# Kernel optimization log

Hardware: AMD Instinct MI355X
Metric: run time of the kernel (lower is better)

## Reference

```python
import jax, jax.numpy as jnp
import numpy as np

NUM_HEADS = 16


def setup_inputs() -> dict:
    key = jax.random.key(0)
    ks = jax.random.split(key, 8)
    b, n, m, L, d = 2, 1024, 4, 1024, 1024
    x = jax.random.normal(ks[0], (b, n, d), dtype=jnp.float32)
    context = jax.random.normal(ks[1], (b, m, L, d), dtype=jnp.float32)
    doc_similarities = jax.random.normal(ks[2], (b, m), dtype=jnp.float32)
    mask = jnp.ones((b, n), dtype=bool)
    context_mask = jnp.ones((b, m, L), dtype=bool)
    Wq = jax.random.normal(ks[3], (d, d), dtype=jnp.float32) * 0.02
    Wkv = jax.random.normal(ks[4], (d, 2 * d), dtype=jnp.float32) * 0.02
    Wout = jax.random.normal(ks[5], (d, d), dtype=jnp.float32) * 0.02
    bout = jnp.zeros((d,), dtype=jnp.float32)
    beta = jnp.ones((), dtype=jnp.float32)
    return {"x": x, "context": context, "doc_similarities": doc_similarities,
            "mask": mask, "context_mask": context_mask,
            "Wq": Wq, "Wkv": Wkv, "Wout": Wout, "bout": bout, "beta": beta}


def reference(x, context, doc_similarities, mask, context_mask, Wq, Wkv, Wout, bout, beta):
    b, n, d = x.shape
    h = NUM_HEADS
    hd = d // h
    _, m, L, _ = context.shape
    kv_len = m * L

    # q projection -> (b, h, n, hd)
    q = (x @ Wq).reshape(b, n, h, hd).transpose(0, 2, 1, 3)

    ctx = context.reshape(b, kv_len, d)
    cmask = context_mask.reshape(b, kv_len)

    # doc similarity bias, broadcast per-token within each doc, scaled by beta
    ds = jnp.repeat(doc_similarities[:, :, None], L, axis=-1).reshape(b, kv_len)
    ds = ds[:, None, None, :] * beta  # (b, 1, 1, kv_len)

    kv = ctx @ Wkv  # (b, kv_len, 2d)
    k, v = jnp.split(kv, 2, axis=-1)
    k = k.reshape(b, kv_len, h, hd).transpose(0, 2, 3, 1)  # (b, h, hd, kv_len)
    v = v.reshape(b, kv_len, h, hd).transpose(0, 2, 1, 3)  # (b, h, kv_len, hd)

    # NOTE: original scales by d**-0.5 (full model dim), not head_size**-0.5
    attention_pre_doc_sim = (q @ k) * (d ** -0.5)  # (b, h, n, kv_len)
    attention = attention_pre_doc_sim + ds

    # faithful mask path: multiply by cross mask, then map exact zeros to -inf
    cross_mask = mask[:, None, :, None] * cmask[:, None, None, :]  # (b,1,n,kv_len)
    attention = attention * cross_mask
    attention = jnp.where(attention == 0.0, -jnp.inf, attention)

    attention_weights = jax.nn.softmax(attention, axis=-1)
    # dropout_rate = 0.0 -> identity

    out = (attention_weights @ v).transpose(0, 2, 1, 3).reshape(b, n, d)
    out = out @ Wout + bout
    return out, attention_pre_doc_sim
```

## Files before the change

kernel.cpp:

```cpp
#include <hip/hip_runtime.h>
#include <cstdint>
#include <cstddef>

typedef unsigned short u16t;
typedef __attribute__((ext_vector_type(4))) float f32x4;
typedef __attribute__((ext_vector_type(4))) int i32x4;
typedef __attribute__((ext_vector_type(8))) __bf16 bf16x8;
typedef __attribute__((ext_vector_type(4))) __bf16 bf16x4;
typedef __attribute__((ext_vector_type(8))) unsigned short u16x8;
typedef __attribute__((ext_vector_type(4))) unsigned short u16x4;

#define INFF __builtin_inff()

__device__ __forceinline__ u16t f2b(float f) {
  union { float f; unsigned u; } x; x.f = f;
  unsigned r = x.u + 0x7FFFu + ((x.u >> 16) & 1u);
  return (u16t)(r >> 16);
}

__device__ __forceinline__ void gload16(const u16t* g, u16t* l) {
  __builtin_amdgcn_global_load_lds((const __attribute__((address_space(1))) void*)g,
                                   (__attribute__((address_space(3))) void*)l, 16, 0, 0);
}

__global__ __launch_bounds__(256) void k_prep(const float* __restrict__ x,
                                              const float* __restrict__ ctx,
                                              u16t* __restrict__ x16,
                                              u16t* __restrict__ ctx16,
                                              const int* __restrict__ cmask,
                                              const float* __restrict__ dsim,
                                              const float* __restrict__ beta_p,
                                              float* __restrict__ biasf) {
  const int bx = blockIdx.x, tid = threadIdx.x;
  if (bx < 2048) {
    int i = bx * 256 + tid;
    f32x4 v = *(const f32x4*)(x + (size_t)i * 4);
    u16x4 o;
    o[0] = f2b(v[0]); o[1] = f2b(v[1]); o[2] = f2b(v[2]); o[3] = f2b(v[3]);
    *(u16x4*)(x16 + (size_t)i * 4) = o;
  } else if (bx < 10240) {
    int i = (bx - 2048) * 256 + tid;
    f32x4 v = *(const f32x4*)(ctx + (size_t)i * 4);
    u16x4 o;
    o[0] = f2b(v[0]); o[1] = f2b(v[1]); o[2] = f2b(v[2]); o[3] = f2b(v[3]);
    *(u16x4*)(ctx16 + (size_t)i * 4) = o;
  } else {
    int idx = (bx - 10240) * 256 + tid;
    int c = idx * 4;
    const float beta = beta_p[0];
    const float ds = dsim[(c >> 12) * 4 + ((c & 4095) >> 10)] * beta;
    i32x4 cm = *(const i32x4*)(cmask + c);
    f32x4 bv;
#pragma unroll
    for (int j = 0; j < 4; ++j) bv[j] = cm[j] ? ds : -INFF;
    *(f32x4*)(biasf + c) = bv;
  }
}

__global__ __launch_bounds__(256) void k_transpose_w3(const float* __restrict__ Wq,
                                                      const float* __restrict__ Wkv,
                                                      const float* __restrict__ Wout,
                                                      u16t* __restrict__ WqT,
                                                      u16t* __restrict__ WkvT,
                                                      u16t* __restrict__ WoutT) {
  __shared__ float tile[64 * 65];
  const int t = threadIdx.x;
  const int bxx = blockIdx.x;
  const float* src; u16t* dst; int C, cb;
  if (bxx < 16)      { src = Wq;   dst = WqT;   C = 1024; cb = bxx * 64; }
  else if (bxx < 48) { src = Wkv;  dst = WkvT;  C = 2048; cb = (bxx - 16) * 64; }
  else               { src = Wout; dst = WoutT; C = 1024; cb = (bxx - 48) * 64; }
  const int rb = blockIdx.y * 64;
#pragma unroll
  for (int it = 0; it < 4; ++it) {
    int c = it * 256 + t;
    int r = c >> 4, ch = c & 15;
    f32x4 v = *(const f32x4*)(src + (size_t)(rb + r) * C + cb + ch * 4);
    float* dp = &tile[r * 65 + ch * 4];
    dp[0] = v[0]; dp[1] = v[1]; dp[2] = v[2]; dp[3] = v[3];
  }
  __syncthreads();
#pragma unroll
  for (int it = 0; it < 2; ++it) {
    int c = it * 256 + t;
    int dr = c >> 3, ch = c & 7;
    u16x8 o;
#pragma unroll
    for (int i = 0; i < 8; ++i) o[i] = f2b(tile[(ch * 8 + i) * 65 + dr]);
    *(u16x8*)(dst + (size_t)(cb + dr) * 1024 + rb + ch * 8) = o;
  }
}

template <int MODE>
__global__ __launch_bounds__(256) void k_gemm_bt(const u16t* __restrict__ A,
                                                 const u16t* __restrict__ Bt,
                                                 void* __restrict__ C,
                                                 u16t* __restrict__ C2,
                                                 const float* __restrict__ bias,
                                                 float oscale,
                                                 int K, int lda, int ldb, int ldc, int nbx) {
  __shared__ u16t As[128 * 64];
  __shared__ u16t Bs[128 * 64];
  const int tid = threadIdx.x;
  const int lane = tid & 63, wid = tid >> 6;
  const int l16 = lane & 15, lg = lane >> 4;
  const int wr = wid >> 1, wc = wid & 1;
  const int g = blockIdx.x, per = gridDim.x >> 3;
  const int w = (g & 7) * per + (g >> 3);
  const int bx = w % nbx, by = w / nbx;
  const int brow = by * 128, bcol = bx * 128;
  const int sr = lane >> 3, chs = lane & 7;
  f32x4 acc[4][4] = {};

  for (int k0 = 0; k0 < K; k0 += 64) {
#pragma unroll
    for (int it = 0; it < 4; ++it) {
      int row = it * 32 + wid * 8 + sr;
      int ch = chs ^ (row & 7);
      gload16(A + (size_t)(brow + row) * lda + k0 + ch * 8, &As[it * 2048 + wid * 512]);
      gload16(Bt + (size_t)(bcol + row) * ldb + k0 + ch * 8, &Bs[it * 2048 + wid * 512]);
    }
    __syncthreads();
#pragma unroll
    for (int kk = 0; kk < 2; ++kk) {
      bf16x8 af[4], bfv[4];
#pragma unroll
      for (int mi = 0; mi < 4; ++mi) {
        int row = wr * 64 + mi * 16 + l16;
        int kch = (kk * 4 + lg) ^ (row & 7);
        af[mi] = *(const bf16x8*)(&As[row * 64 + kch * 8]);
      }
#pragma unroll
      for (int ni = 0; ni < 4; ++ni) {
        int row = wc * 64 + ni * 16 + l16;
        int kch = (kk * 4 + lg) ^ (row & 7);
        bfv[ni] = *(const bf16x8*)(&Bs[row * 64 + kch * 8]);
      }
#pragma unroll
      for (int mi = 0; mi < 4; ++mi)
#pragma unroll
        for (int ni = 0; ni < 4; ++ni)
          acc[mi][ni] = __builtin_amdgcn_mfma_f32_16x16x32_bf16(af[mi], bfv[ni], acc[mi][ni], 0, 0, 0);
    }
    __syncthreads();
  }

  if (MODE == 2 && bcol >= 1024) {
#pragma unroll
    for (int mi = 0; mi < 4; ++mi) {
#pragma unroll
      for (int ni = 0; ni < 4; ++ni) {
        int vcol = bcol - 1024 + wc * 64 + ni * 16 + l16;
        int h = vcol >> 6, hd = vcol & 63;
        int row0 = brow + wr * 64 + mi * 16 + lg * 4;
        int bb = row0 >> 12, pos = row0 & 4095;
        u16x4 o4;
#pragma unroll
        for (int j = 0; j < 4; ++j) o4[j] = f2b(acc[mi][ni][j]);
        *(u16x4*)(C2 + ((size_t)((bb * 16 + h) * 64 + hd)) * 4096 + pos) = o4;
      }
    }
    return;
  }
#pragma unroll
  for (int mi = 0; mi < 4; ++mi) {
#pragma unroll
    for (int ni = 0; ni < 4; ++ni) {
#pragma unroll
      for (int j = 0; j < 4; ++j) {
        size_t row = (size_t)brow + wr * 64 + mi * 16 + lg * 4 + j;
        int col = bcol + wc * 64 + ni * 16 + l16;
        float v = acc[mi][ni][j] * oscale;
        if (MODE == 1) {
          v += bias[col];
          __builtin_nontemporal_store(v, (float*)C + row * ldc + col);
        } else {
          ((u16t*)C)[row * ldc + col] = f2b(v);
        }
      }
    }
  }
}

__global__ __launch_bounds__(256) void k_attn(const u16t* __restrict__ k16,
                                              const u16t* __restrict__ vT16,
                                              const u16t* __restrict__ q16,
                                              const float* __restrict__ biasf,
                                              const int* __restrict__ mask,
                                              float* __restrict__ pre,
                                              u16t* __restrict__ O16) {
  __shared__ u16t Ks[2][128 * 64];
  __shared__ u16t Vs[2][64 * 128];
  __shared__ u16t Ps[4 * 16 * 128];

  const int tid = threadIdx.x;
  const int lane = tid & 63, wid = tid >> 6;
  const int l16 = lane & 15, lg = lane >> 4;
  const int g = blockIdx.x;
  const int w = (g & 7) * 64 + (g >> 3);
  const int nb = w & 15, hb = w >> 4;
  const int h = hb & 15, b = hb >> 4;
  const int qrow0 = nb * 64 + wid * 16;

  bf16x8 aq0, aq1;
  {
    const u16t* qp = q16 + (size_t)(b * 1024 + qrow0 + l16) * 1024 + h * 64 + lg * 8;
    aq0 = *(const bf16x8*)(qp);
    aq1 = *(const bf16x8*)(qp + 32);
  }
  const bool qm = mask[b * 1024 + qrow0 + l16] != 0;

  float mrow = -INFF, lsum = 0.f;
  f32x4 o[4] = {};

  const u16t* kbase = k16 + (size_t)b * 4096 * 1024 + (size_t)h * 64;
  const u16t* vbase = vT16 + (size_t)(b * 16 + h) * 64 * 4096;
  float* prerow = pre + (size_t)((b * 16 + h) * 1024 + qrow0 + l16) * 4096;
  const float* biasb = biasf + b * 4096;
  u16t* Pw = &Ps[wid * 2048];
  char* Pwb = (char*)Pw + l16 * 256;
  const int pswz = (l16 & 7) << 4;

  auto stage = [&](int bufi, int kv0s) {
    u16t* Kb = &Ks[bufi][wid * 2048];
    u16t* Vb = &Vs[bufi][wid * 2048];
#pragma unroll
    for (int it = 0; it < 4; ++it) {
      int row = wid * 32 + it * 8 + (lane >> 3);
      int ch = (lane & 7) ^ (row & 7);
      gload16(kbase + (size_t)(kv0s + row) * 1024 + ch * 8, Kb + it * 512);
    }
#pragma unroll
    for (int it = 0; it < 4; ++it) {
      int row = wid * 16 + it * 4 + (lane >> 4);
      int ch = (lane & 15) ^ (row & 7);
      gload16(vbase + (size_t)row * 4096 + kv0s + ch * 8, Vb + it * 512);
    }
  };

  int cur = 0;
  stage(0, 0);
  __syncthreads();

  for (int t = 0; t < 32; ++t) {
    if (t + 1 < 32) stage(cur ^ 1, (t + 1) * 128);
    asm volatile("" ::: "memory");
    const u16t* Kc = &Ks[cur][0];
    const u16t* Vc = &Vs[cur][0];
    const int kv0 = t * 128;

    f32x4 s[8];
#pragma unroll
    for (int kb = 0; kb < 8; ++kb) {
      f32x4 acc = {0.f, 0.f, 0.f, 0.f};
      int row = kb * 16 + l16;
      bf16x8 bk0 = *(const bf16x8*)(&Kc[row * 64 + ((lg ^ (row & 7)) << 3)]);
      bf16x8 bk1 = *(const bf16x8*)(&Kc[row * 64 + (((4 + lg) ^ (row & 7)) << 3)]);
      acc = __builtin_amdgcn_mfma_f32_16x16x32_bf16(bk0, aq0, acc, 0, 0, 0);
      acc = __builtin_amdgcn_mfma_f32_16x16x32_bf16(bk1, aq1, acc, 0, 0, 0);
      s[kb] = acc;
    }

    float tmax = -INFF;
#pragma unroll
    for (int kb = 0; kb < 8; ++kb) {
      const int colb = kv0 + kb * 16 + lg * 4;
      __builtin_nontemporal_store(s[kb], (f32x4*)(prerow + colb));
      f32x4 bv = *(const f32x4*)(biasb + colb);
#pragma unroll
      for (int j = 0; j < 4; ++j) {
        float t2 = s[kb][j] + bv[j];
        if (!qm) t2 = 0.f;
        if (t2 == 0.f) t2 = -INFF;
        s[kb][j] = t2;
        tmax = fmaxf(tmax, t2);
      }
    }
    tmax = fmaxf(tmax, __shfl_xor(tmax, 16, 64));
    tmax = fmaxf(tmax, __shfl_xor(tmax, 32, 64));
    const float mold = mrow;
    const float mn = fmaxf(mold, tmax);
    const bool nochange = __all(mn == mold);
    mrow = mn;

    float psum = 0.f;
#pragma unroll
    for (int kb = 0; kb < 8; ++kb) {
      bf16x4 pb;
#pragma unroll
      for (int j = 0; j < 4; ++j) {
        float p = (mn == -INFF) ? 0.f : __expf(s[kb][j] - mn);
        psum += p;
        pb[j] = (__bf16)p;
      }
      *(bf16x4*)(Pwb + ((kb * 32 + lg * 8) ^ pswz)) = pb;
    }
    asm volatile("" ::: "memory");
    psum += __shfl_xor(psum, 16, 64);
    psum += __shfl_xor(psum, 32, 64);

    if (nochange) {
      lsum += psum;
    } else {
      const float fs = (mn == -INFF) ? 0.f : __expf(mold - mn);
      lsum = lsum * fs + psum;
      float fsj[4];
#pragma unroll
      for (int j = 0; j < 4; ++j) fsj[j] = __shfl(fs, lg * 4 + j, 64);
#pragma unroll
      for (int ni = 0; ni < 4; ++ni)
#pragma unroll
        for (int j = 0; j < 4; ++j) o[ni][j] *= fsj[j];
    }

#pragma unroll
    for (int kk2 = 0; kk2 < 4; ++kk2) {
      bf16x8 pa = *(const bf16x8*)(Pwb + ((kk2 * 64 + lg * 16) ^ pswz));
#pragma unroll
      for (int ni = 0; ni < 4; ++ni) {
        int vrow = ni * 16 + l16;
        bf16x8 vb = *(const bf16x8*)(&Vc[vrow * 128 + (((kk2 * 4 + lg) ^ (vrow & 7)) << 3)]);
        o[ni] = __builtin_amdgcn_mfma_f32_16x16x32_bf16(pa, vb, o[ni], 0, 0, 0);
      }
    }

    asm volatile("s_waitcnt vmcnt(8) lgkmcnt(0)" ::: "memory");
    __builtin_amdgcn_sched_barrier(0);
    __builtin_amdgcn_s_barrier();
    __builtin_amdgcn_sched_barrier(0);
    cur ^= 1;
  }

  float lsj[4];
#pragma unroll
  for (int j = 0; j < 4; ++j) lsj[j] = __shfl(lsum, lg * 4 + j, 64);
#pragma unroll
  for (int ni = 0; ni < 4; ++ni) {
#pragma unroll
    for (int j = 0; j < 4; ++j) {
      size_t row = (size_t)b * 1024 + qrow0 + lg * 4 + j;
      int col = h * 64 + ni * 16 + l16;
      O16[row * 1024 + col] = f2b(o[ni][j] / lsj[j]);
    }
  }
}

extern "C" void kernel_launch(void* const* d_in, const int* in_sizes, int n_in,
                              void* d_out, int out_size, void* d_ws, size_t ws_size,
                              hipStream_t stream) {
  const float* x = (const float*)d_in[0];
  const float* ctx = (const float*)d_in[1];
  const float* dsim = (const float*)d_in[2];
  const int* mask = (const int*)d_in[3];
  const int* cmask = (const int*)d_in[4];
  const float* Wq = (const float*)d_in[5];
  const float* Wkv = (const float*)d_in[6];
  const float* Wout = (const float*)d_in[7];
  const float* bout = (const float*)d_in[8];
  const float* beta = (const float*)d_in[9];

  char* ws = (char*)d_ws;
  u16t* q16 = (u16t*)(ws + (0ull << 20));
  u16t* k16 = (u16t*)(ws + (4ull << 20));
  u16t* vT16 = (u16t*)(ws + (36ull << 20));
  u16t* O16 = (u16t*)(ws + (52ull << 20));
  u16t* x16 = (u16t*)(ws + (56ull << 20));
  u16t* ctx16 = (u16t*)(ws + (60ull << 20));
  u16t* WqT = (u16t*)(ws + (76ull << 20));
  u16t* WkvT = (u16t*)(ws + (78ull << 20));
  u16t* WoutT = (u16t*)(ws + (82ull << 20));
  float* biasf = (float*)(ws + (84ull << 20));

  float* outp = (float*)d_out;
  float* pre = outp + (size_t)2 * 1024 * 1024;

  k_prep<<<10248, 256, 0, stream>>>(x, ctx, x16, ctx16, cmask, dsim, beta, biasf);
  k_transpose_w3<<<dim3(64, 16), 256, 0, stream>>>(Wq, Wkv, Wout, WqT, WkvT, WoutT);

  k_gemm_bt<0><<<128, 256, 0, stream>>>(x16, WqT, (void*)q16, nullptr, nullptr, 0.03125f, 1024, 1024, 1024, 1024, 8);
  k_gemm_bt<2><<<1024, 256, 0, stream>>>(ctx16, WkvT, (void*)k16, vT16, nullptr, 1.0f, 1024, 1024, 1024, 1024, 16);
  k_attn<<<512, 256, 0, stream>>>(k16, vT16, q16, biasf, mask, pre, O16);
  k_gemm_bt<1><<<128, 256, 0, stream>>>(O16, WoutT, d_out, nullptr, bout, 1.0f, 1024, 1024, 1024, 1024, 8);
}
```

Before: 261.9 us.

## Process two query tiles per wave in attention and pack context mask into bits

Each attention wave now handles 32 query rows (two 16-row tiles) against the same staged K/V tiles, halving the grid to 256 blocks and doubling reuse of each K/V load from shared memory. The float bias array is replaced by a packed bitmask of the context mask plus per-doc similarity computed in-kernel, cutting bias-load traffic. s_setprio hints are added around MFMA sections. This raises register pressure and leaves fewer blocks than CUs, which risks lower occupancy and underused hardware.

Measured after the change: 273.4 us. 4.4% more time.

```diff
diff --git a/kernel.cpp b/kernel.cpp
--- a/kernel.cpp
+++ b/kernel.cpp
@@ -5,6 +5,7 @@
 typedef unsigned short u16t;
 typedef __attribute__((ext_vector_type(4))) float f32x4;
 typedef __attribute__((ext_vector_type(4))) int i32x4;
+typedef __attribute__((ext_vector_type(4))) unsigned int u32x4;
 typedef __attribute__((ext_vector_type(8))) __bf16 bf16x8;
 typedef __attribute__((ext_vector_type(4))) __bf16 bf16x4;
 typedef __attribute__((ext_vector_type(8))) unsigned short u16x8;
@@ -28,9 +29,7 @@
                                               u16t* __restrict__ x16,
                                               u16t* __restrict__ ctx16,
                                               const int* __restrict__ cmask,
-                                              const float* __restrict__ dsim,
-                                              const float* __restrict__ beta_p,
-                                              float* __restrict__ biasf) {
+                                              unsigned int* __restrict__ cmbits) {
   const int bx = blockIdx.x, tid = threadIdx.x;
   if (bx < 2048) {
     int i = bx * 256 + tid;
@@ -45,15 +44,12 @@
     o[0] = f2b(v[0]); o[1] = f2b(v[1]); o[2] = f2b(v[2]); o[3] = f2b(v[3]);
     *(u16x4*)(ctx16 + (size_t)i * 4) = o;
   } else {
-    int idx = (bx - 10240) * 256 + tid;
-    int c = idx * 4;
-    const float beta = beta_p[0];
-    const float ds = dsim[(c >> 12) * 4 + ((c & 4095) >> 10)] * beta;
-    i32x4 cm = *(const i32x4*)(cmask + c);
-    f32x4 bv;
-#pragma unroll
-    for (int j = 0; j < 4; ++j) bv[j] = cm[j] ? ds : -INFF;
-    *(f32x4*)(biasf + c) = bv;
+    int b = tid >> 7, wdi = tid & 127;
+    const int* cp = cmask + b * 4096 + wdi * 32;
+    unsigned int bits = 0;
+#pragma unroll
+    for (int i = 0; i < 32; ++i) bits |= (cp[i] != 0 ? 1u : 0u) << i;
+    cmbits[tid] = bits;
   }
 }
 
@@ -185,7 +181,9 @@
 __global__ __launch_bounds__(256) void k_attn(const u16t* __restrict__ k16,
                                               const u16t* __restrict__ vT16,
                                               const u16t* __restrict__ q16,
-                                              const float* __restrict__ biasf,
+                                              const unsigned int* __restrict__ cmbits,
+                                              const float* __restrict__ dsim,
+                                              const float* __restrict__ beta_p,
                                               const int* __restrict__ mask,
                                               float* __restrict__ pre,
                                               u16t* __restrict__ O16) {
@@ -197,26 +195,34 @@
   const int lane = tid & 63, wid = tid >> 6;
   const int l16 = lane & 15, lg = lane >> 4;
   const int g = blockIdx.x;
-  const int w = (g & 7) * 64 + (g >> 3);
-  const int nb = w & 15, hb = w >> 4;
+  const int w = (g & 7) * 32 + (g >> 3);
+  const int nb = w & 7, hb = w >> 3;
   const int h = hb & 15, b = hb >> 4;
-  const int qrow0 = nb * 64 + wid * 16;
-
-  bf16x8 aq0, aq1;
+  const int qrow0 = nb * 128 + wid * 32;
+
+  bf16x8 aqA0, aqA1, aqB0, aqB1;
   {
     const u16t* qp = q16 + (size_t)(b * 1024 + qrow0 + l16) * 1024 + h * 64 + lg * 8;
-    aq0 = *(const bf16x8*)(qp);
-    aq1 = *(const bf16x8*)(qp + 32);
-  }
-  const bool qm = mask[b * 1024 + qrow0 + l16] != 0;
-
-  float mrow = -INFF, lsum = 0.f;
-  f32x4 o[4] = {};
+    aqA0 = *(const bf16x8*)(qp);
+    aqA1 = *(const bf16x8*)(qp + 32);
+    aqB0 = *(const bf16x8*)(qp + 16 * 1024);
+    aqB1 = *(const bf16x8*)(qp + 16 * 1024 + 32);
+  }
+  const bool qmA = mask[b * 1024 + qrow0 + l16] != 0;
+  const bool qmB = mask[b * 1024 + qrow0 + 16 + l16] != 0;
+
+  const float beta = beta_p[0];
+  const float ds40 = dsim[b * 4 + 0] * beta, ds41 = dsim[b * 4 + 1] * beta;
+  const float ds42 = dsim[b * 4 + 2] * beta, ds43 = dsim[b * 4 + 3] * beta;
+
+  float mrowA = -INFF, lsumA = 0.f, mrowB = -INFF, lsumB = 0.f;
+  f32x4 oA[4] = {}, oB[4] = {};
 
   const u16t* kbase = k16 + (size_t)b * 4096 * 1024 + (size_t)h * 64;
   const u16t* vbase = vT16 + (size_t)(b * 16 + h) * 64 * 4096;
-  float* prerow = pre + (size_t)((b * 16 + h) * 1024 + qrow0 + l16) * 4096;
-  const float* biasb = biasf + b * 4096;
+  float* prerowA = pre + (size_t)((b * 16 + h) * 1024 + qrow0 + l16) * 4096;
+  float* prerowB = prerowA + (size_t)16 * 4096;
+  const u32x4* cmw = (const u32x4*)(cmbits + b * 128);
   u16t* Pw = &Ps[wid * 2048];
   char* Pwb = (char*)Pw + l16 * 256;
   const int pswz = (l16 & 7) << 4;
@@ -238,58 +244,70 @@
     }
   };
 
+  u32x4 Wc = cmw[0];
   int cur = 0;
   stage(0, 0);
   __syncthreads();
 
   for (int t = 0; t < 32; ++t) {
-    if (t + 1 < 32) stage(cur ^ 1, (t + 1) * 128);
+    u32x4 Wn = Wc;
+    if (t + 1 < 32) {
+      Wn = cmw[t + 1];
+      stage(cur ^ 1, (t + 1) * 128);
+    }
     asm volatile("" ::: "memory");
     const u16t* Kc = &Ks[cur][0];
     const u16t* Vc = &Vs[cur][0];
     const int kv0 = t * 128;
-
-    f32x4 s[8];
+    const int d = t >> 3;
+    const float ds_t = (d & 1) ? ((d & 2) ? ds43 : ds41) : ((d & 2) ? ds42 : ds40);
+
+    f32x4 sA[8], sB[8];
+    __builtin_amdgcn_s_setprio(1);
 #pragma unroll
     for (int kb = 0; kb < 8; ++kb) {
-      f32x4 acc = {0.f, 0.f, 0.f, 0.f};
       int row = kb * 16 + l16;
       bf16x8 bk0 = *(const bf16x8*)(&Kc[row * 64 + ((lg ^ (row & 7)) << 3)]);
       bf16x8 bk1 = *(const bf16x8*)(&Kc[row * 64 + (((4 + lg) ^ (row & 7)) << 3)]);
-      acc = __builtin_amdgcn_mfma_f32_16x16x32_bf16(bk0, aq0, acc, 0, 0, 0);
-      acc = __builtin_amdgcn_mfma_f32_16x16x32_bf16(bk1, aq1, acc, 0, 0, 0);
-      s[kb] = acc;
-    }
+      f32x4 a0 = {0.f, 0.f, 0.f, 0.f};
+      a0 = __builtin_amdgcn_mfma_f32_16x16x32_bf16(bk0, aqA0, a0, 0, 0, 0);
+      a0 = __builtin_amdgcn_mfma_f32_16x16x32_bf16(bk1, aqA1, a0, 0, 0, 0);
+      sA[kb] = a0;
+      f32x4 b0 = {0.f, 0.f, 0.f, 0.f};
+      b0 = __builtin_amdgcn_mfma_f32_16x16x32_bf16(bk0, aqB0, b0, 0, 0, 0);
+      b0 = __builtin_amdgcn_mfma_f32_16x16x32_bf16(bk1, aqB1, b0, 0, 0, 0);
+      sB[kb] = b0;
+    }
+    __builtin_amdgcn_s_setprio(0);
 
     float tmax = -INFF;
 #pragma unroll
     for (int kb = 0; kb < 8; ++kb) {
-      const int colb = kv0 + kb * 16 + lg * 4;
-      __builtin_nontemporal_store(s[kb], (f32x4*)(prerow + colb));
-      f32x4 bv = *(const f32x4*)(biasb + colb);
+      const int cb2 = kv0 + kb * 16 + lg * 4;
+      __builtin_nontemporal_store(sA[kb], (f32x4*)(prerowA + cb2));
+      const unsigned int sh = Wc[kb >> 1] >> ((kb & 1) * 16 + lg * 4);
 #pragma unroll
       for (int j = 0; j < 4; ++j) {
-        float t2 = s[kb][j] + bv[j];
-        if (!qm) t2 = 0.f;
+        float bias = ((sh >> j) & 1u) ? ds_t : -INFF;
+        float t2 = sA[kb][j] + bias;
+        if (!qmA) t2 = 0.f;
         if (t2 == 0.f) t2 = -INFF;
-        s[kb][j] = t2;
+        sA[kb][j] = t2;
         tmax = fmaxf(tmax, t2);
       }
     }
     tmax = fmaxf(tmax, __shfl_xor(tmax, 16, 64));
     tmax = fmaxf(tmax, __shfl_xor(tmax, 32, 64));
-    const float mold = mrow;
-    const float mn = fmaxf(mold, tmax);
-    const bool nochange = __all(mn == mold);
-    mrow = mn;
-
+    const float moldA = mrowA;
+    const float mnA = fmaxf(moldA, tmax);
+    mrowA = mnA;
     float psum = 0.f;
 #pragma unroll
     for (int kb = 0; kb < 8; ++kb) {
       bf16x4 pb;
 #pragma unroll
       for (int j = 0; j < 4; ++j) {
-        float p = (mn == -INFF) ? 0.f : __expf(s[kb][j] - mn);
+        float p = (mnA == -INFF) ? 0.f : __expf(sA[kb][j] - mnA);
         psum += p;
         pb[j] = (__bf16)p;
       }
@@ -298,50 +316,117 @@
     asm volatile("" ::: "memory");
     psum += __shfl_xor(psum, 16, 64);
     psum += __shfl_xor(psum, 32, 64);
-
-    if (nochange) {
-      lsum += psum;
+    if (__all(mnA == moldA)) {
+      lsumA += psum;
     } else {
-      const float fs = (mn == -INFF) ? 0.f : __expf(mold - mn);
-      lsum = lsum * fs + psum;
-      float fsj[4];
-#pragma unroll
-      for (int j = 0; j < 4; ++j) fsj[j] = __shfl(fs, lg * 4 + j, 64);
-#pragma unroll
-      for (int ni = 0; ni < 4; ++ni)
-#pragma unroll
-        for (int j = 0; j < 4; ++j) o[ni][j] *= fsj[j];
-    }
-
+      const float fs = (mnA == -INFF) ? 0.f : __expf(moldA - mnA);
+      lsumA = lsumA * fs + psum;
+      float f0 = __shfl(fs, lg * 4 + 0, 64), f1 = __shfl(fs, lg * 4 + 1, 64);
+      float f2 = __shfl(fs, lg * 4 + 2, 64), f3 = __shfl(fs, lg * 4 + 3, 64);
+#pragma unroll
+      for (int ni = 0; ni < 4; ++ni) {
+        oA[ni][0] *= f0; oA[ni][1] *= f1; oA[ni][2] *= f2; oA[ni][3] *= f3;
+      }
+    }
+    bf16x8 paA0 = *(const bf16x8*)(Pwb + ((0 * 64 + lg * 16) ^ pswz));
+    bf16x8 paA1 = *(const bf16x8*)(Pwb + ((1 * 64 + lg * 16) ^ pswz));
+    bf16x8 paA2 = *(const bf16x8*)(Pwb + ((2 * 64 + lg * 16) ^ pswz));
+    bf16x8 paA3 = *(const bf16x8*)(Pwb + ((3 * 64 + lg * 16) ^ pswz));
+    asm volatile("" ::: "memory");
+
+    tmax = -INFF;
+#pragma unroll
+    for (int kb = 0; kb < 8; ++kb) {
+      const int cb2 = kv0 + kb * 16 + lg * 4;
+      __builtin_nontemporal_store(sB[kb], (f32x4*)(prerowB + cb2));
+      const unsigned int sh = Wc[kb >> 1] >> ((kb & 1) * 16 + lg * 4);
+#pragma unroll
+      for (int j = 0; j < 4; ++j) {
+        float bias = ((sh >> j) & 1u) ? ds_t : -INFF;
+        float t2 = sB[kb][j] + bias;
+        if (!qmB) t2 = 0.f;
+        if (t2 == 0.f) t2 = -INFF;
+        sB[kb][j] = t2;
+        tmax = fmaxf(tmax, t2);
+      }
+    }
+    tmax = fmaxf(tmax, __shfl_xor(tmax, 16, 64));
+    tmax = fmaxf(tmax, __shfl_xor(tmax, 32, 64));
+    const float moldB = mrowB;
+    const float mnB = fmaxf(moldB, tmax);
+    mrowB = mnB;
+    psum = 0.f;
+#pragma unroll
+    for (int kb = 0; kb < 8; ++kb) {
+      bf16x4 pb;
+#pragma unroll
+      for (int j = 0; j < 4; ++j) {
+        float p = (mnB == -INFF) ? 0.f : __expf(sB[kb][j] - mnB);
+        psum += p;
+        pb[j] = (__bf16)p;
+      }
+      *(bf16x4*)(Pwb + ((kb * 32 + lg * 8) ^ pswz)) = pb;
+    }
+    asm volatile("" ::: "memory");
+    psum += __shfl_xor(psum, 16, 64);
+    psum += __shfl_xor(psum, 32, 64);
+    if (__all(mnB == moldB)) {
+      lsumB += psum;
+    } else {
+      const float fs = (mnB == -INFF) ? 0.f : __expf(moldB - mnB);
+      lsumB = lsumB * fs + psum;
+      float f0 = __shfl(fs, lg * 4 + 0, 64), f1 = __shfl(fs, lg * 4 + 1, 64);
+      float f2 = __shfl(fs, lg * 4 + 2, 64), f3 = __shfl(fs, lg * 4 + 3, 64);
+#pragma unroll
+      for (int ni = 0; ni < 4; ++ni) {
+        oB[ni][0] *= f0; oB[ni][1] *= f1; oB[ni][2] *= f2; oB[ni][3] *= f3;
+      }
+    }
+    bf16x8 paB0 = *(const bf16x8*)(Pwb + ((0 * 64 + lg * 16) ^ pswz));
+    bf16x8 paB1 = *(const bf16x8*)(Pwb + ((1 * 64 + lg * 16) ^ pswz));
+    bf16x8 paB2 = *(const bf16x8*)(Pwb + ((2 * 64 + lg * 16) ^ pswz));
+    bf16x8 paB3 = *(const bf16x8*)(Pwb + ((3 * 64 + lg * 16) ^ pswz));
+
+    __builtin_amdgcn_s_setprio(1);
 #pragma unroll
     for (int kk2 = 0; kk2 < 4; ++kk2) {
-      bf16x8 pa = *(const bf16x8*)(Pwb + ((kk2 * 64 + lg * 16) ^ pswz));
+      bf16x8 pa_a = (kk2 == 0) ? paA0 : (kk2 == 1) ? paA1 : (kk2 == 2) ? paA2 : paA3;
+      bf16x8 pa_b = (kk2 == 0) ? paB0 : (kk2 == 1) ? paB1 : (kk2 == 2) ? paB2 : paB3;
 #pragma unroll
       for (int ni = 0; ni < 4; ++ni) {
         int vrow = ni * 16 + l16;
         bf16x8 vb = *(const bf16x8*)(&Vc[vrow * 128 + (((kk2 * 4 + lg) ^ (vrow & 7)) << 3)]);
-        o[ni] = __builtin_amdgcn_mfma_f32_16x16x32_bf16(pa, vb, o[ni], 0, 0, 0);
-      }
-    }
-
-    asm volatile("s_waitcnt vmcnt(8) lgkmcnt(0)" ::: "memory");
+        oA[ni] = __builtin_amdgcn_mfma_f32_16x16x32_bf16(pa_a, vb, oA[ni], 0, 0, 0);
+        oB[ni] = __builtin_amdgcn_mfma_f32_16x16x32_bf16(pa_b, vb, oB[ni], 0, 0, 0);
+      }
+    }
+    __builtin_amdgcn_s_setprio(0);
+
+    asm volatile("s_waitcnt vmcnt(16) lgkmcnt(0)" ::: "memory");
     __builtin_amdgcn_sched_barrier(0);
     __builtin_amdgcn_s_barrier();
     __builtin_amdgcn_sched_barrier(0);
+    Wc = Wn;
     cur ^= 1;
   }
 
-  float lsj[4];
-#pragma unroll
-  for (int j = 0; j < 4; ++j) lsj[j] = __shfl(lsum, lg * 4 + j, 64);
+  float lsA0 = __shfl(lsumA, lg * 4 + 0, 64), lsA1 = __shfl(lsumA, lg * 4 + 1, 64);
+  float lsA2 = __shfl(lsumA, lg * 4 + 2, 64), lsA3 = __shfl(lsumA, lg * 4 + 3, 64);
+  float lsB0 = __shfl(lsumB, lg * 4 + 0, 64), lsB1 = __shfl(lsumB, lg * 4 + 1, 64);
+  float lsB2 = __shfl(lsumB, lg * 4 + 2, 64), lsB3 = __shfl(lsumB, lg * 4 + 3, 64);
 #pragma unroll
   for (int ni = 0; ni < 4; ++ni) {
-#pragma unroll
-    for (int j = 0; j < 4; ++j) {
-      size_t row = (size_t)b * 1024 + qrow0 + lg * 4 + j;
-      int col = h * 64 + ni * 16 + l16;
-      O16[row * 1024 + col] = f2b(o[ni][j] / lsj[j]);
-    }
+    size_t rowA = (size_t)b * 1024 + qrow0 + lg * 4;
+    int col = h * 64 + ni * 16 + l16;
+    O16[(rowA + 0) * 1024 + col] = f2b(oA[ni][0] / lsA0);
+    O16[(rowA + 1) * 1024 + col] = f2b(oA[ni][1] / lsA1);
+    O16[(rowA + 2) * 1024 + col] = f2b(oA[ni][2] / lsA2);
+    O16[(rowA + 3) * 1024 + col] = f2b(oA[ni][3] / lsA3);
+    size_t rowB = rowA + 16;
+    O16[(rowB + 0) * 1024 + col] = f2b(oB[ni][0] / lsB0);
+    O16[(rowB + 1) * 1024 + col] = f2b(oB[ni][1] / lsB1);
+    O16[(rowB + 2) * 1024 + col] = f2b(oB[ni][2] / lsB2);
+    O16[(rowB + 3) * 1024 + col] = f2b(oB[ni][3] / lsB3);
   }
 }
 
@@ -369,16 +454,16 @@
   u16t* WqT = (u16t*)(ws + (76ull << 20));
   u16t* WkvT = (u16t*)(ws + (78ull << 20));
   u16t* WoutT = (u16t*)(ws + (82ull << 20));
-  float* biasf = (float*)(ws + (84ull << 20));
+  unsigned int* cmbits = (unsigned int*)(ws + (84ull << 20));
 
   float* outp = (float*)d_out;
   float* pre = outp + (size_t)2 * 1024 * 1024;
 
-  k_prep<<<10248, 256, 0, stream>>>(x, ctx, x16, ctx16, cmask, dsim, beta, biasf);
+  k_prep<<<10241, 256, 0, stream>>>(x, ctx, x16, ctx16, cmask, cmbits);
   k_transpose_w3<<<dim3(64, 16), 256, 0, stream>>>(Wq, Wkv, Wout, WqT, WkvT, WoutT);
 
   k_gemm_bt<0><<<128, 256, 0, stream>>>(x16, WqT, (void*)q16, nullptr, nullptr, 0.03125f, 1024, 1024, 1024, 1024, 8);
   k_gemm_bt<2><<<1024, 256, 0, stream>>>(ctx16, WkvT, (void*)k16, vT16, nullptr, 1.0f, 1024, 1024, 1024, 1024, 16);
-  k_attn<<<512, 256, 0, stream>>>(k16, vT16, q16, biasf, mask, pre, O16);
+  k_attn<<<256, 256, 0, stream>>>(k16, vT16, q16, cmbits, dsim, beta, mask, pre, O16);
   k_gemm_bt<1><<<128, 256, 0, stream>>>(O16, WoutT, d_out, nullptr, bout, 1.0f, 1024, 1024, 1024, 1024, 8);
 }
```
